# Kernel optimization log

Measured on AMD Instinct MI355X. Metric: run time of the kernel, lower is better.

Reference implementation:

```python
import jax, jax.numpy as jnp
import numpy as np

C = 256        # channels per FPN level (in_channels == representation_size)
PATCH = 5      # GNN kernel_size == stride
NEG_SLOPE = 0.2
K = 7          # node_connectivities[0]


def _conv1x1(x, w, b):
    return jnp.einsum('bchw,oc->bohw', x, w) + b[None, :, None, None]


def _conv3x3(x, w, b):
    y = jax.lax.conv_general_dilated(x, w, (1, 1), 'SAME',
                                     dimension_numbers=('NCHW', 'OIHW', 'NCHW'))
    return y + b[None, :, None, None]


def _nearest(x, hout, wout):
    hin, win = x.shape[-2:]
    ih = (jnp.arange(hout) * hin) // hout
    iw = (jnp.arange(wout) * win) // wout
    return x[..., ih, :][..., iw]


def _topk_edges(score, k, n):
    # torch: A.scatter(1, topk_idx, topk_val); edge = nonzero(triu(A)); edge=[col,row]
    vals, idx = jax.lax.top_k(score, k)          # per-row top-k
    row = jnp.repeat(jnp.arange(n), k)
    col = idx.reshape(-1)
    val = vals.reshape(-1)
    # triu keeps col>=row; GATv2Conv removes self loops then re-adds one per node
    mask = (col > row) & (val != 0.0)
    loop = jnp.arange(n)
    src = jnp.concatenate([col, loop])           # PyG edge_index[0] = source
    dst = jnp.concatenate([row, loop])
    emask = jnp.concatenate([mask, jnp.ones((n,), bool)])
    return src, dst, emask


def _gatv2(x, src, dst, emask, wl, bl, wr, br, att, bias, n):
    heads, dout = att.shape
    xl = (x @ wl + bl).reshape(n, heads, dout)   # source transform (lin_l)
    xr = (x @ wr + br).reshape(n, heads, dout)   # target transform (lin_r)
    m = xl[src] + xr[dst]                        # [E, H, D]
    e = jnp.sum(jax.nn.leaky_relu(m, NEG_SLOPE) * att[None], axis=-1)  # [E, H]
    e = jnp.where(emask[:, None], e, -1e30)
    emax = jax.ops.segment_max(e, dst, num_segments=n)
    w = jnp.exp(e - emax[dst]) * emask[:, None]
    denom = jax.ops.segment_sum(w, dst, num_segments=n)
    alpha = w / (denom[dst] + 1e-16)
    out = jax.ops.segment_sum(alpha[..., None] * xl[src], dst, num_segments=n)
    return out.reshape(n, heads * dout) + bias


def _gnn(x, p, k):
    # x: [1, C, H, W], H,W divisible by PATCH
    _, c, hh, ww = x.shape
    nh, nw = hh // PATCH, ww // PATCH
    n = nh * nw
    patches = x[0].reshape(c, nh, PATCH, nw, PATCH).transpose(1, 3, 0, 2, 4)
    patches = patches.reshape(n, c, PATCH, PATCH)
    emb = jax.nn.relu(jnp.einsum('ncij,ocij->no', patches, p['conv1_w']) + p['conv1_b'])
    emb = jax.nn.relu(emb @ p['fc2_w'].T + p['fc2_b'])
    # feature-similarity kNN graph
    src, dst, em = _topk_edges(emb @ emb.T, k, n)
    h = jax.nn.elu(_gatv2(emb, src, dst, em, *p['g1'], n))
    h = jax.nn.elu(_gatv2(h, src, dst, em, *p['g2'], n))
    # spatial kNN graph (k smallest distances; self distance 0 drops out via val!=0)
    ii, jj = jnp.meshgrid(jnp.arange(nh) * PATCH, jnp.arange(nw) * PATCH, indexing='ij')
    centers = jnp.stack([ii.reshape(-1), jj.reshape(-1)], -1).astype(x.dtype)
    dist = jnp.sqrt(jnp.sum((centers[:, None] - centers[None]) ** 2, -1))
    src2, dst2, em2 = _topk_edges(-dist, k, n)
    h2 = jax.nn.elu(_gatv2(emb, src2, dst2, em2, *p['g3'], n))
    h2 = jax.nn.elu(_gatv2(h2, src2, dst2, em2, *p['g4'], n))
    hc = jax.nn.relu(jnp.concatenate([h, h2], 1) @ p['fc3_w'].T + p['fc3_b']) + h2
    # torch: reshape(dim,dim,C).swapdims(-1,0) -> [C, nw, nh]
    grid = jnp.transpose(hc.reshape(nh, nw, c), (2, 1, 0))
    # ConvTranspose2d(C, C, 5, stride=5): non-overlapping tiling
    up = jnp.einsum('cij,coab->oiajb', grid, p['convT_w'])
    up = up.reshape(c, nw * PATCH, nh * PATCH) + p['convT_b'][:, None, None]
    return jax.nn.relu(up)[None]


def _forward(feat0, feat1, inner_w, inner_b, layer_w, layer_b, convT_w, convT_b,
             conv1_w, conv1_b, fc2_w, fc2_b, fc3_w, fc3_b,
             g1_wl, g1_bl, g1_wr, g1_br, g1_att, g1_bias,
             g2_wl, g2_bl, g2_wr, g2_br, g2_att, g2_bias,
             g3_wl, g3_bl, g3_wr, g3_br, g3_att, g3_bias,
             g4_wl, g4_bl, g4_wr, g4_br, g4_att, g4_bias, k):
    feats = [feat0, feat1]
    xs = []
    for i, f in enumerate(feats):
        p = dict(conv1_w=conv1_w[i], conv1_b=conv1_b[i],
                 fc2_w=fc2_w[i], fc2_b=fc2_b[i],
                 fc3_w=fc3_w[i], fc3_b=fc3_b[i],
                 convT_w=convT_w[i], convT_b=convT_b[i],
                 g1=(g1_wl[i], g1_bl[i], g1_wr[i], g1_br[i], g1_att[i], g1_bias[i]),
                 g2=(g2_wl[i], g2_bl[i], g2_wr[i], g2_br[i], g2_att[i], g2_bias[i]),
                 g3=(g3_wl[i], g3_bl[i], g3_wr[i], g3_br[i], g3_att[i], g3_bias[i]),
                 g4=(g4_wl[i], g4_bl[i], g4_wr[i], g4_br[i], g4_att[i], g4_bias[i]))
        xs.append(f + _gnn(f, p, k))
    # top-down FPN
    last = _conv1x1(xs[1], inner_w[1], inner_b[1])
    out1 = _conv3x3(last, layer_w[1], layer_b[1])
    inner0 = _conv1x1(xs[0], inner_w[0], inner_b[0])
    td = _nearest(last, xs[0].shape[-2], xs[0].shape[-1])
    out0 = _conv3x3(inner0 + td, layer_w[0], layer_b[0])
    return out0, out1


def setup_inputs() -> dict:
    key = jax.random.key(0)
    keys = jax.random.split(key, 48)
    it = iter(range(48))
    def rn(shape, s=0.05):
        return (jax.random.normal(keys[next(it)], shape) * s).astype(jnp.float32)
    H8 = 8 * C
    inp = dict(
        feat0=rn((1, C, 200, 200), 1.0),
        feat1=rn((1, C, 100, 100), 1.0),
        inner_w=rn((2, C, C)), inner_b=rn((2, C)),
        layer_w=rn((2, C, C, 3, 3)), layer_b=rn((2, C)),
        convT_w=rn((2, C, C, PATCH, PATCH)), convT_b=rn((2, C)),
        conv1_w=rn((2, C, C, PATCH, PATCH)), conv1_b=rn((2, C)),
        fc2_w=rn((2, C, C)), fc2_b=rn((2, C)),
        fc3_w=rn((2, C, 2 * C)), fc3_b=rn((2, C)),
        g1_wl=rn((2, C, H8)), g1_bl=rn((2, H8)), g1_wr=rn((2, C, H8)), g1_br=rn((2, H8)),
        g1_att=rn((2, 8, C)), g1_bias=rn((2, H8)),
        g2_wl=rn((2, H8, C)), g2_bl=rn((2, C)), g2_wr=rn((2, H8, C)), g2_br=rn((2, C)),
        g2_att=rn((2, 1, C)), g2_bias=rn((2, C)),
        g3_wl=rn((2, C, H8)), g3_bl=rn((2, H8)), g3_wr=rn((2, C, H8)), g3_br=rn((2, H8)),
        g3_att=rn((2, 8, C)), g3_bias=rn((2, H8)),
        g4_wl=rn((2, H8, C)), g4_bl=rn((2, C)), g4_wr=rn((2, H8, C)), g4_br=rn((2, C)),
        g4_att=rn((2, 1, C)), g4_bias=rn((2, C)),
        k=K,
    )
    return inp


def reference(feat0, feat1, inner_w, inner_b, layer_w, layer_b, convT_w, convT_b,
              conv1_w, conv1_b, fc2_w, fc2_b, fc3_w, fc3_b,
              g1_wl, g1_bl, g1_wr, g1_br, g1_att, g1_bias,
              g2_wl, g2_bl, g2_wr, g2_br, g2_att, g2_bias,
              g3_wl, g3_bl, g3_wr, g3_br, g3_att, g3_bias,
              g4_wl, g4_bl, g4_wr, g4_br, g4_att, g4_bias, k):
    return _forward(feat0, feat1, inner_w, inner_b, layer_w, layer_b, convT_w, convT_b,
                    conv1_w, conv1_b, fc2_w, fc2_b, fc3_w, fc3_b,
                    g1_wl, g1_bl, g1_wr, g1_br, g1_att, g1_bias,
                    g2_wl, g2_bl, g2_wr, g2_br, g2_att, g2_bias,
                    g3_wl, g3_bl, g3_wr, g3_br, g3_att, g3_bias,
                    g4_wl, g4_bl, g4_wr, g4_br, g4_att, g4_bias, k)
```

## Files before the change

### kernel.cpp

```cpp
#include <hip/hip_runtime.h>
#include <cstdint>
#include <cstddef>
#include <math.h>

#define KNN 7

using short8  = __attribute__((ext_vector_type(8))) short;
using floatx4 = __attribute__((ext_vector_type(4))) float;

static const size_t OFF_ARENA = 0;
static const size_t OFF_XS0   = 10240000;
static const size_t OFF_XS1   = 20480000;
static const size_t OFF_LAST  = 23040000;
static const size_t OFF_EMB   = 25600000;
static const size_t OFF_EMB2  = 26009600;
static const size_t OFF_XL    = 26419200;
static const size_t OFF_H1    = 32972800;
static const size_t OFF_XL2   = 36249600;
static const size_t OFF_CAT   = 37068800;
static const size_t OFF_HC    = 37888000;
static const size_t OFF_SRCF  = 38400000;
static const size_t OFF_SRCS  = 38411200;
static const size_t OFF_BF_A  = 38422400;
static const size_t OFF_BF_W  = 40122400;

static __device__ __forceinline__ unsigned short f2bf(float f) {
    union { float f; unsigned u; } v; v.f = f;
    unsigned u = v.u;
    unsigned r = u + 0x7fffu + ((u >> 16) & 1u);
    return (unsigned short)(r >> 16);
}

template<int ACT, bool BIAS>
__global__ __launch_bounds__(256)
void gemm_k(const float* __restrict__ A, const float* __restrict__ B,
            const float* __restrict__ bias, float* __restrict__ C, int M, int N, int K)
{
    __shared__ float As[16][68];
    __shared__ float Bs[16][68];
    const int tid = threadIdx.x;
    const int bm0 = blockIdx.y * 64;
    const int bn0 = blockIdx.x * 64;
    const int tx = tid & 15, ty = tid >> 4;
    const int lrow = tid >> 2;
    const int lk4  = (tid & 3) << 2;
    const int m = bm0 + lrow;
    const int nn = bn0 + lrow;
    const bool aok = m < M, bok = nn < N;
    float acc[4][4] = {{0.f,0.f,0.f,0.f},{0.f,0.f,0.f,0.f},{0.f,0.f,0.f,0.f},{0.f,0.f,0.f,0.f}};

    float4 va = {0.f,0.f,0.f,0.f}, vb = {0.f,0.f,0.f,0.f};
    if (aok) va = *(const float4*)(A + (size_t)m * K + lk4);
    if (bok) vb = *(const float4*)(B + (size_t)nn * K + lk4);

    for (int k0 = 0; k0 < K; k0 += 16) {
        As[lk4+0][lrow]=va.x; As[lk4+1][lrow]=va.y; As[lk4+2][lrow]=va.z; As[lk4+3][lrow]=va.w;
        Bs[lk4+0][lrow]=vb.x; Bs[lk4+1][lrow]=vb.y; Bs[lk4+2][lrow]=vb.z; Bs[lk4+3][lrow]=vb.w;
        __syncthreads();
        float4 na = {0.f,0.f,0.f,0.f}, nb = {0.f,0.f,0.f,0.f};
        const bool more = (k0 + 16) < K;
        if (more) {
            if (aok) na = *(const float4*)(A + (size_t)m * K + (k0 + 16 + lk4));
            if (bok) nb = *(const float4*)(B + (size_t)nn * K + (k0 + 16 + lk4));
        }
        #pragma unroll
        for (int k = 0; k < 16; k++) {
            const float4 av = *(const float4*)&As[k][ty << 2];
            const float4 bv = *(const float4*)&Bs[k][tx << 2];
            const float a0=av.x,a1=av.y,a2=av.z,a3=av.w;
            const float b0=bv.x,b1=bv.y,b2=bv.z,b3=bv.w;
            acc[0][0]=fmaf(a0,b0,acc[0][0]); acc[0][1]=fmaf(a0,b1,acc[0][1]);
            acc[0][2]=fmaf(a0,b2,acc[0][2]); acc[0][3]=fmaf(a0,b3,acc[0][3]);
            acc[1][0]=fmaf(a1,b0,acc[1][0]); acc[1][1]=fmaf(a1,b1,acc[1][1]);
            acc[1][2]=fmaf(a1,b2,acc[1][2]); acc[1][3]=fmaf(a1,b3,acc[1][3]);
            acc[2][0]=fmaf(a2,b0,acc[2][0]); acc[2][1]=fmaf(a2,b1,acc[2][1]);
            acc[2][2]=fmaf(a2,b2,acc[2][2]); acc[2][3]=fmaf(a2,b3,acc[2][3]);
            acc[3][0]=fmaf(a3,b0,acc[3][0]); acc[3][1]=fmaf(a3,b1,acc[3][1]);
            acc[3][2]=fmaf(a3,b2,acc[3][2]); acc[3][3]=fmaf(a3,b3,acc[3][3]);
        }
        __syncthreads();
        va = na; vb = nb;
    }
    #pragma unroll
    for (int i = 0; i < 4; i++) {
        const int mm = bm0 + (ty << 2) + i;
        if (mm >= M) continue;
        #pragma unroll
        for (int jj = 0; jj < 4; jj++) {
            const int nc = bn0 + (tx << 2) + jj;
            if (nc >= N) continue;
            float v = acc[i][jj];
            if (BIAS) v += bias[nc];
            if (ACT == 1) v = fmaxf(v, 0.f);
            C[(size_t)mm * N + nc] = v;
        }
    }
}

template<int ACT, bool BIAS>
static inline void gemm32(hipStream_t s, const float* A, const float* B, const float* bias,
                          float* C, int M, int N, int K)
{
    dim3 g((N + 63) / 64, (M + 63) / 64);
    gemm_k<ACT, BIAS><<<g, dim3(256), 0, s>>>(A, B, bias, C, M, N, K);
}

__global__ __launch_bounds__(256)
void gemm32_sk_k(const float* __restrict__ A, const float* __restrict__ B,
                 float* __restrict__ part, int M, int N, int K, int Kc)
{
    __shared__ float As[16][68];
    __shared__ float Bs[16][68];
    const int tid = threadIdx.x;
    const int bm0 = blockIdx.y * 64;
    const int bn0 = blockIdx.x * 64;
    const int sblk = blockIdx.z;
    const int kbeg = sblk * Kc;
    const int kend = (kbeg + Kc < K) ? kbeg + Kc : K;
    const int tx = tid & 15, ty = tid >> 4;
    const int lrow = tid >> 2;
    const int lk4  = (tid & 3) << 2;
    const int m = bm0 + lrow;
    const int nn = bn0 + lrow;
    const bool aok = m < M, bok = nn < N;
    float acc[4][4] = {{0.f,0.f,0.f,0.f},{0.f,0.f,0.f,0.f},{0.f,0.f,0.f,0.f},{0.f,0.f,0.f,0.f}};

    float4 va = {0.f,0.f,0.f,0.f}, vb = {0.f,0.f,0.f,0.f};
    if (aok) va = *(const float4*)(A + (size_t)m * K + kbeg + lk4);
    if (bok) vb = *(const float4*)(B + (size_t)nn * K + kbeg + lk4);

    for (int k0 = kbeg; k0 < kend; k0 += 16) {
        As[lk4+0][lrow]=va.x; As[lk4+1][lrow]=va.y; As[lk4+2][lrow]=va.z; As[lk4+3][lrow]=va.w;
        Bs[lk4+0][lrow]=vb.x; Bs[lk4+1][lrow]=vb.y; Bs[lk4+2][lrow]=vb.z; Bs[lk4+3][lrow]=vb.w;
        __syncthreads();
        float4 na = {0.f,0.f,0.f,0.f}, nb = {0.f,0.f,0.f,0.f};
        const bool more = (k0 + 16) < kend;
        if (more) {
            if (aok) na = *(const float4*)(A + (size_t)m * K + (k0 + 16 + lk4));
            if (bok) nb = *(const float4*)(B + (size_t)nn * K + (k0 + 16 + lk4));
        }
        #pragma unroll
        for (int k = 0; k < 16; k++) {
            const float4 av = *(const float4*)&As[k][ty << 2];
            const float4 bv = *(const float4*)&Bs[k][tx << 2];
            const float a0=av.x,a1=av.y,a2=av.z,a3=av.w;
            const float b0=bv.x,b1=bv.y,b2=bv.z,b3=bv.w;
            acc[0][0]=fmaf(a0,b0,acc[0][0]); acc[0][1]=fmaf(a0,b1,acc[0][1]);
            acc[0][2]=fmaf(a0,b2,acc[0][2]); acc[0][3]=fmaf(a0,b3,acc[0][3]);
            acc[1][0]=fmaf(a1,b0,acc[1][0]); acc[1][1]=fmaf(a1,b1,acc[1][1]);
            acc[1][2]=fmaf(a1,b2,acc[1][2]); acc[1][3]=fmaf(a1,b3,acc[1][3]);
            acc[2][0]=fmaf(a2,b0,acc[2][0]); acc[2][1]=fmaf(a2,b1,acc[2][1]);
            acc[2][2]=fmaf(a2,b2,acc[2][2]); acc[2][3]=fmaf(a2,b3,acc[2][3]);
            acc[3][0]=fmaf(a3,b0,acc[3][0]); acc[3][1]=fmaf(a3,b1,acc[3][1]);
            acc[3][2]=fmaf(a3,b2,acc[3][2]); acc[3][3]=fmaf(a3,b3,acc[3][3]);
        }
        __syncthreads();
        va = na; vb = nb;
    }
    float* P = part + (size_t)sblk * M * N;
    #pragma unroll
    for (int i = 0; i < 4; i++) {
        const int mm = bm0 + (ty << 2) + i;
        if (mm >= M) continue;
        #pragma unroll
        for (int jj = 0; jj < 4; jj++) {
            const int nc = bn0 + (tx << 2) + jj;
            if (nc >= N) continue;
            P[(size_t)mm * N + nc] = acc[i][jj];
        }
    }
}

template<int ACT, bool BIAS>
__global__ void sk_reduce_k(const float* __restrict__ part, const float* __restrict__ bias,
                            float* __restrict__ C, int MN, int N, int S)
{
    const int i4 = (blockIdx.x * 256 + threadIdx.x) * 4;
    if (i4 >= MN) return;
    float4 a = *(const float4*)(part + i4);
    for (int s = 1; s < S; s++) {
        const float4 b = *(const float4*)(part + (size_t)s * MN + i4);
        a.x += b.x; a.y += b.y; a.z += b.z; a.w += b.w;
    }
    if (BIAS) {
        const int n = i4 % N;
        a.x += bias[n]; a.y += bias[n + 1]; a.z += bias[n + 2]; a.w += bias[n + 3];
    }
    if (ACT == 1) {
        a.x = fmaxf(a.x, 0.f); a.y = fmaxf(a.y, 0.f);
        a.z = fmaxf(a.z, 0.f); a.w = fmaxf(a.w, 0.f);
    }
    *(float4*)(C + i4) = a;
}

template<int ACT, bool BIAS>
static inline void gemm32_sk(hipStream_t s, const float* A, const float* B, const float* bias,
                             float* C, float* part, int M, int N, int K, int S)
{
    const int Kc = ((K / S + 15) / 16) * 16;
    dim3 g((N + 63) / 64, (M + 63) / 64, S);
    gemm32_sk_k<<<g, dim3(256), 0, s>>>(A, B, part, M, N, K, Kc);
    const int MN = M * N;
    sk_reduce_k<ACT, BIAS><<<dim3((MN / 4 + 255) / 256), dim3(256), 0, s>>>(part, bias, C, MN, N, S);
}

enum { BT_NT = 0, BT_CONV2 = 2 };

template<int BT, int ACT, int BAX, bool ADDMAT>
__global__ __launch_bounds__(256)
void bgemm_k(const unsigned short* __restrict__ A, const unsigned short* __restrict__ B,
             const float* __restrict__ bias, const float* __restrict__ bias2, int nsplit,
             const float* __restrict__ Dmat, int Dld,
             float* __restrict__ C, int M, int N, int K, int imH, int imW)
{
    __shared__ unsigned short Asl[128][40];
    __shared__ unsigned short Bsl[128][40];
    const int tid  = threadIdx.x;
    const int lane = tid & 63;
    const int wid  = tid >> 6;
    const int quad = lane >> 4;
    const int l15  = lane & 15;
    const int wy = wid >> 1, wx = wid & 1;
    const int bm0 = blockIdx.y * 128;
    const int bn0 = blockIdx.x * 128;

    floatx4 zero = {0.f, 0.f, 0.f, 0.f};
    floatx4 acc[4][4];
    #pragma unroll
    for (int i = 0; i < 4; i++)
        #pragma unroll
        for (int j = 0; j < 4; j++) acc[i][j] = zero;

    const int srow = tid >> 1;
    const int skc  = (tid & 1) << 4;
    const int mrow = bm0 + srow;
    const bool aok = mrow < M;
    const int nrow = bn0 + srow;
    const bool bok = nrow < N;

    int cy = 0, cx = 0; bool cok = false;
    if (BT == BT_CONV2) {
        cok = nrow < N;
        const int pp = cok ? nrow : 0;
        cy = pp / imW; cx = pp - cy * imW;
    }

    auto loadA = [&](int k0, uint4& r0, uint4& r1) {
        r0 = (uint4){0,0,0,0}; r1 = (uint4){0,0,0,0};
        if (aok) {
            const uint4* p = (const uint4*)(A + (size_t)mrow * K + k0 + skc);
            r0 = p[0]; r1 = p[1];
        }
    };
    auto loadB = [&](int k0, uint4& r0, uint4& r1) {
        r0 = (uint4){0,0,0,0}; r1 = (uint4){0,0,0,0};
        if (BT == BT_NT) {
            if (bok) {
                const uint4* p = (const uint4*)(B + (size_t)nrow * K + k0 + skc);
                r0 = p[0]; r1 = p[1];
            }
        } else {
            const int jj = k0 >> 8;
            const int j3 = jj / 3;
            const int dy = j3 - 1, dx = jj - j3 * 3 - 1;
            const int c0 = k0 & 255;
            const int yy = cy + dy, xx = cx + dx;
            if (cok && (unsigned)yy < (unsigned)imH && (unsigned)xx < (unsigned)imW) {
                const uint4* p = (const uint4*)(B + ((size_t)yy * imW + xx) * 256 + c0 + skc);
                r0 = p[0]; r1 = p[1];
            }
        }
    };
    auto stage = [&](const uint4& a0, const uint4& a1, const uint4& b0, const uint4& b1) {
        *(uint4*)&Asl[srow][skc]     = a0;
        *(uint4*)&Asl[srow][skc + 8] = a1;
        *(uint4*)&Bsl[srow][skc]     = b0;
        *(uint4*)&Bsl[srow][skc + 8] = b1;
    };
    auto compute = [&]() {
        short8 af[4], bfr[4];
        #pragma unroll
        for (int i = 0; i < 4; i++)
            af[i] = *(const short8*)&Asl[wy * 64 + i * 16 + l15][quad * 8];
        #pragma unroll
        for (int j = 0; j < 4; j++)
            bfr[j] = *(const short8*)&Bsl[wx * 64 + j * 16 + l15][quad * 8];
        #pragma unroll
        for (int i = 0; i < 4; i++)
            #pragma unroll
            for (int j = 0; j < 4; j++)
                acc[i][j] = __builtin_amdgcn_mfma_f32_16x16x32_bf16(af[i], bfr[j], acc[i][j], 0, 0, 0);
    };

    uint4 a00, a01, b00, b01, a10, a11, b10, b11;
    loadA(0, a00, a01); loadB(0, b00, b01);
    if (32 < K) { loadA(32, a10, a11); loadB(32, b10, b11); }

    for (int k0 = 0; k0 < K; k0 += 64) {
        stage(a00, a01, b00, b01);
        __syncthreads();
        if (k0 + 64 < K) { loadA(k0 + 64, a00, a01); loadB(k0 + 64, b00, b01); }
        compute();
        __syncthreads();
        if (k0 + 32 < K) {
            stage(a10, a11, b10, b11);
            __syncthreads();
            if (k0 + 96 < K) { loadA(k0 + 96, a10, a11); loadB(k0 + 96, b10, b11); }
            compute();
            __syncthreads();
        }
    }

    #pragma unroll
    for (int i = 0; i < 4; i++) {
        #pragma unroll
        for (int r = 0; r < 4; r++) {
            const int m = bm0 + wy * 64 + i * 16 + quad * 4 + r;
            if (m >= M) continue;
            #pragma unroll
            for (int j = 0; j < 4; j++) {
                const int n = bn0 + wx * 64 + j * 16 + l15;
                if (n >= N) continue;
                float v = acc[i][j][r];
                if (bias != nullptr)
                    v += (BAX == 0) ? bias[m] : (n < nsplit ? bias[n] : bias2[n - nsplit]);
                if (ACT == 1) v = fmaxf(v, 0.f);
                if (ADDMAT) v += Dmat[(size_t)m * Dld + n];
                C[(size_t)m * N + n] = v;
            }
        }
    }
}

template<int BT, int ACT, int BAX, bool ADDMAT>
static inline void bgemm(hipStream_t s, const unsigned short* A, const unsigned short* B,
                         const float* bias, const float* bias2, int nsplit,
                         const float* D, int Dld, float* C,
                         int M, int N, int K, int imH = 0, int imW = 0)
{
    dim3 g((N + 127) / 128, (M + 127) / 128);
    bgemm_k<BT, ACT, BAX, ADDMAT><<<g, dim3(256), 0, s>>>(A, B, bias, bias2, nsplit,
                                                          D, Dld, C, M, N, K, imH, imW);
}

__global__ __launch_bounds__(256)
void bgemm_sk_k(const unsigned short* __restrict__ A, const unsigned short* __restrict__ B,
                float* __restrict__ part, int M, int N, int K, int Kc)
{
    __shared__ unsigned short Asl[128][40];
    __shared__ unsigned short Bsl[128][40];
    const int tid  = threadIdx.x;
    const int lane = tid & 63;
    const int wid  = tid >> 6;
    const int quad = lane >> 4;
    const int l15  = lane & 15;
    const int wy = wid >> 1, wx = wid & 1;
    const int bm0 = blockIdx.y * 128;
    const int bn0 = blockIdx.x * 128;
    const int kbeg = blockIdx.z * Kc;
    const int kend = (kbeg + Kc < K) ? kbeg + Kc : K;

    floatx4 zero = {0.f, 0.f, 0.f, 0.f};
    floatx4 acc[4][4];
    #pragma unroll
    for (int i = 0; i < 4; i++)
        #pragma unroll
        for (int j = 0; j < 4; j++) acc[i][j] = zero;

    const int srow = tid >> 1;
    const int skc  = (tid & 1) << 4;
    const int mrow = bm0 + srow;
    const bool aok = mrow < M;
    const int nrow = bn0 + srow;
    const bool bok = nrow < N;

    auto loadA = [&](int k0, uint4& r0, uint4& r1) {
        r0 = (uint4){0,0,0,0}; r1 = (uint4){0,0,0,0};
        if (aok) {
            const uint4* p = (const uint4*)(A + (size_t)mrow * K + k0 + skc);
            r0 = p[0]; r1 = p[1];
        }
    };
    auto loadB = [&](int k0, uint4& r0, uint4& r1) {
        r0 = (uint4){0,0,0,0}; r1 = (uint4){0,0,0,0};
        if (bok) {
            const uint4* p = (const uint4*)(B + (size_t)nrow * K + k0 + skc);
            r0 = p[0]; r1 = p[1];
        }
    };
    auto stage = [&](const uint4& a0, const uint4& a1, const uint4& b0, const uint4& b1) {
        *(uint4*)&Asl[srow][skc]     = a0;
        *(uint4*)&Asl[srow][skc + 8] = a1;
        *(uint4*)&Bsl[srow][skc]     = b0;
        *(uint4*)&Bsl[srow][skc + 8] = b1;
    };
    auto compute = [&]() {
        short8 af[4], bfr[4];
        #pragma unroll
        for (int i = 0; i < 4; i++)
            af[i] = *(const short8*)&Asl[wy * 64 + i * 16 + l15][quad * 8];
        #pragma unroll
        for (int j = 0; j < 4; j++)
            bfr[j] = *(const short8*)&Bsl[wx * 64 + j * 16 + l15][quad * 8];
        #pragma unroll
        for (int i = 0; i < 4; i++)
            #pragma unroll
            for (int j = 0; j < 4; j++)
                acc[i][j] = __builtin_amdgcn_mfma_f32_16x16x32_bf16(af[i], bfr[j], acc[i][j], 0, 0, 0);
    };

    uint4 a00, a01, b00, b01, a10, a11, b10, b11;
    loadA(kbeg, a00, a01); loadB(kbeg, b00, b01);
    if (kbeg + 32 < kend) { loadA(kbeg + 32, a10, a11); loadB(kbeg + 32, b10, b11); }

    for (int k0 = kbeg; k0 < kend; k0 += 64) {
        stage(a00, a01, b00, b01);
        __syncthreads();
        if (k0 + 64 < kend) { loadA(k0 + 64, a00, a01); loadB(k0 + 64, b00, b01); }
        compute();
        __syncthreads();
        if (k0 + 32 < kend) {
            stage(a10, a11, b10, b11);
            __syncthreads();
            if (k0 + 96 < kend) { loadA(k0 + 96, a10, a11); loadB(k0 + 96, b10, b11); }
            compute();
            __syncthreads();
        }
    }

    float* P = part + (size_t)blockIdx.z * M * N;
    #pragma unroll
    for (int i = 0; i < 4; i++) {
        #pragma unroll
        for (int r = 0; r < 4; r++) {
            const int m = bm0 + wy * 64 + i * 16 + quad * 4 + r;
            if (m >= M) continue;
            #pragma unroll
            for (int j = 0; j < 4; j++) {
                const int n = bn0 + wx * 64 + j * 16 + l15;
                if (n >= N) continue;
                P[(size_t)m * N + n] = acc[i][j][r];
            }
        }
    }
}

template<int ACT, bool ADDMAT>
__global__ void bsk_reduce_k(const float* __restrict__ part,
                             const float* __restrict__ bias, const float* __restrict__ bias2,
                             int nsplit, const float* __restrict__ Dmat, int Dld,
                             float* __restrict__ C, int MN, int N, int S)
{
    const int i4 = (blockIdx.x * 256 + threadIdx.x) * 4;
    if (i4 >= MN) return;
    float4 a = *(const float4*)(part + i4);
    for (int s = 1; s < S; s++) {
        const float4 b = *(const float4*)(part + (size_t)s * MN + i4);
        a.x += b.x; a.y += b.y; a.z += b.z; a.w += b.w;
    }
    const int n = i4 % N;
    const float* bb = (n < nsplit) ? (bias + n) : (bias2 + n - nsplit);
    a.x += bb[0]; a.y += bb[1]; a.z += bb[2]; a.w += bb[3];
    if (ACT == 1) {
        a.x = fmaxf(a.x, 0.f); a.y = fmaxf(a.y, 0.f);
        a.z = fmaxf(a.z, 0.f); a.w = fmaxf(a.w, 0.f);
    }
    if (ADDMAT) {
        const int m = i4 / N;
        const float4 d = *(const float4*)(Dmat + (size_t)m * Dld + n);
        a.x += d.x; a.y += d.y; a.z += d.z; a.w += d.w;
    }
    *(float4*)(C + i4) = a;
}

template<int ACT, bool ADDMAT>
static inline void bgemm_sk(hipStream_t s, const unsigned short* A, const unsigned short* B,
                            const float* bias, const float* bias2, int nsplit,
                            const float* D, int Dld, float* C, float* part,
                            int M, int N, int K, int S)
{
    const int Kc = ((K / S + 31) / 32) * 32;
    dim3 g((N + 127) / 128, (M + 127) / 128, S);
    bgemm_sk_k<<<g, dim3(256), 0, s>>>(A, B, part, M, N, K, Kc);
    const int MN = M * N;
    bsk_reduce_k<ACT, ADDMAT><<<dim3((MN / 4 + 255) / 256), dim3(256), 0, s>>>(
        part, bias, bias2, nsplit, D, Dld, C, MN, N, S);
}

__global__ void cast_bf16_k(const float* __restrict__ in, unsigned short* __restrict__ out, int total)
{
    const int i4 = (blockIdx.x * 256 + threadIdx.x) * 4;
    if (i4 + 4 <= total) {
        const float4 v = *(const float4*)(in + i4);
        ushort4 o;
        o.x = f2bf(v.x); o.y = f2bf(v.y); o.z = f2bf(v.z); o.w = f2bf(v.w);
        *(ushort4*)(out + i4) = o;
    } else {
        for (int i = i4; i < total; i++) out[i] = f2bf(in[i]);
    }
}

static inline void cast_bf(hipStream_t s, const float* in, unsigned short* out, int total)
{
    cast_bf16_k<<<dim3((total / 4 + 255) / 256), dim3(256), 0, s>>>(in, out, total);
}

__device__ __forceinline__ void cast_t_body(const float* __restrict__ in,
                                            unsigned short* __restrict__ out, int K, int N)
{
    __shared__ float tile[64][65];
    const int n0 = blockIdx.x * 64;
    const int k0 = blockIdx.y * 64;
    const int t = threadIdx.x;
    const int r = t >> 2;
    const int c4 = (t & 3) << 4;
    {
        const int k = k0 + r;
        if (k < K && n0 + c4 + 16 <= N) {
            const float4* p = (const float4*)(in + (size_t)k * N + n0 + c4);
            *(float4*)&tile[r][c4]      = p[0];
            *(float4*)&tile[r][c4 + 4]  = p[1];
            *(float4*)&tile[r][c4 + 8]  = p[2];
            *(float4*)&tile[r][c4 + 12] = p[3];
        } else {
            for (int i = 0; i < 16; i++)
                tile[r][c4 + i] = (k < K && n0 + c4 + i < N) ? in[(size_t)k * N + n0 + c4 + i] : 0.f;
        }
    }
    __syncthreads();
    const int n = n0 + r;
    if (n >= N) return;
    unsigned short tmp[16];
    #pragma unroll
    for (int i = 0; i < 16; i++) tmp[i] = f2bf(tile[c4 + i][r]);
    if (k0 + 64 <= K) {
        *(uint4*)(out + (size_t)n * K + k0 + c4)     = *(uint4*)&tmp[0];
        *(uint4*)(out + (size_t)n * K + k0 + c4 + 8) = *(uint4*)&tmp[8];
    } else {
        for (int i = 0; i < 16; i++)
            if (k0 + c4 + i < K) out[(size_t)n * K + k0 + c4 + i] = tmp[i];
    }
}

__global__ void cast_t_k(const float* __restrict__ in, unsigned short* __restrict__ out, int K, int N)
{
    cast_t_body(in, out, K, N);
}

__global__ void cast_t2_k(const float* __restrict__ in0, const float* __restrict__ in1,
                          unsigned short* __restrict__ out0, unsigned short* __restrict__ out1,
                          int K, int N)
{
    if (blockIdx.z == 0) cast_t_body(in0, out0, K, N);
    else                 cast_t_body(in1, out1, K, N);
}

static inline void cast_t(hipStream_t s, const float* in, unsigned short* out, int K, int N)
{
    cast_t_k<<<dim3((N + 63) / 64, (K + 63) / 64), dim3(256), 0, s>>>(in, out, K, N);
}

static inline void cast_t2(hipStream_t s, const float* in0, const float* in1,
                           unsigned short* out0, unsigned short* out1, int K, int N)
{
    cast_t2_k<<<dim3((N + 63) / 64, (K + 63) / 64, 2), dim3(256), 0, s>>>(in0, in1, out0, out1, K, N);
}

__global__ void reorder_w3_k(const float* __restrict__ in, unsigned short* __restrict__ out)
{
    const int idx = blockIdx.x * 256 + threadIdx.x;
    if (idx >= 589824) return;
    const int o = idx / 2304;
    const int r = idx - o * 2304;
    const int j = r >> 8;
    const int c = r & 255;
    out[idx] = f2bf(in[(size_t)o * 2304 + c * 9 + j]);
}

__global__ void extract_patches_k(const float* __restrict__ f, float* __restrict__ patches,
                                  int nw, int H, int total)
{
    int idx = blockIdx.x * 256 + threadIdx.x;
    if (idx >= total) return;
    int q = idx % 6400;
    int p = idx / 6400;
    int c = q / 25;
    int rem = q - c * 25;
    int a = rem / 5, b = rem - (rem / 5) * 5;
    int ih = p / nw, iw = p - (p / nw) * nw;
    patches[idx] = f[(size_t)c * H * H + (size_t)(ih * 5 + a) * H + (iw * 5 + b)];
}

__global__ void topk_feat_k(const float* __restrict__ score, int* __restrict__ srcCols, int n)
{
    const int r = blockIdx.x;
    const int lane = threadIdx.x;
    const float* row = score + (size_t)r * n;
    int   sel[KNN];
    float selv[KNN];
    #pragma unroll
    for (int t = 0; t < KNN; t++) {
        float best = -__builtin_huge_valf();
        int   bidx = 0x7fffffff;
        for (int c = lane; c < n; c += 64) {
            bool taken = false;
            #pragma unroll
            for (int u = 0; u < KNN; u++)
                if (u < t && sel[u] == c) taken = true;
            if (taken) continue;
            float v = row[c];
            if (v > best || (v == best && c < bidx)) { best = v; bidx = c; }
        }
        #pragma unroll
        for (int off = 32; off > 0; off >>= 1) {
            float ov = __shfl_down(best, off);
            int   oi = __shfl_down(bidx, off);
            if (ov > best || (ov == best && oi < bidx)) { best = ov; bidx = oi; }
        }
        best = __shfl(best, 0);
        bidx = __shfl(bidx, 0);
        sel[t] = bidx; selv[t] = best;
    }
    if (lane < KNN) {
        int c = -1; float v = 0.f;
        #pragma unroll
        for (int t = 0; t < KNN; t++)
            if (lane == t) { c = sel[t]; v = selv[t]; }
        srcCols[r * KNN + lane] = (c > r && v != 0.0f) ? c : -1;
    }
}

__global__ void topk_spatial_k(int* __restrict__ srcCols, int n, int nw)
{
    const int r = blockIdx.x;
    const int lane = threadIdx.x;
    const int ri = r / nw, rj = r - (r / nw) * nw;
    int sel[KNN];
    #pragma unroll
    for (int t = 0; t < KNN; t++) {
        int bkey = 0x7fffffff;
        for (int c = lane; c < n; c += 64) {
            bool taken = false;
            #pragma unroll
            for (int u = 0; u < KNN; u++)
                if (u < t && sel[u] == c) taken = true;
            if (taken) continue;
            const int ci = c / nw, cj = c - (c / nw) * nw;
            const int dy = (ri - ci) * 5, dx = (rj - cj) * 5;
            const int d2 = dy * dy + dx * dx;
            const int key = (d2 << 11) | c;
            if (key < bkey) bkey = key;
        }
        #pragma unroll
        for (int off = 32; off > 0; off >>= 1) {
            int ok = __shfl_down(bkey, off);
            if (ok < bkey) bkey = ok;
        }
        bkey = __shfl(bkey, 0);
        sel[t] = bkey & 2047;
    }
    if (lane < KNN) {
        int c = -1;
        #pragma unroll
        for (int t = 0; t < KNN; t++) if (lane == t) c = sel[t];
        srcCols[r * KNN + lane] = (c > r) ? c : -1;
    }
}

__global__ void gat_fused_k(const float* __restrict__ x, int xroff, int xstride,
                            const float* __restrict__ att,
                            const int* __restrict__ srcCols, const float* __restrict__ bias,
                            float* __restrict__ out, int n, int H, int ostride, int ooff)
{
    const int wid = (blockIdx.x * blockDim.x + threadIdx.x) >> 6;
    const int lane = threadIdx.x & 63;
    if (wid >= n * H) return;
    const int h = wid % H;
    const int r = wid / H;
    const int d0 = lane << 2;

    const float4 xrf  = *(const float4*)(x + (size_t)r * xstride + xroff + h * 256 + d0);
    const float4 attf = *(const float4*)(att + (size_t)h * 256 + d0);

    int srcs[8];
    #pragma unroll
    for (int s_ = 0; s_ < KNN; s_++) srcs[s_] = srcCols[r * KNN + s_];
    srcs[7] = r;

    float4 xlf[8];
    float  e[8];
    #pragma unroll
    for (int s_ = 0; s_ < 8; s_++) {
        const int c = srcs[s_];
        float4 v = {0.f, 0.f, 0.f, 0.f};
        if (c >= 0) v = *(const float4*)(x + (size_t)c * xstride + h * 256 + d0);
        xlf[s_] = v;
        float m, p = 0.f;
        m = v.x + xrf.x; m = (m > 0.f) ? m : 0.2f * m; p += m * attf.x;
        m = v.y + xrf.y; m = (m > 0.f) ? m : 0.2f * m; p += m * attf.y;
        m = v.z + xrf.z; m = (m > 0.f) ? m : 0.2f * m; p += m * attf.z;
        m = v.w + xrf.w; m = (m > 0.f) ? m : 0.2f * m; p += m * attf.w;
        #pragma unroll
        for (int off = 32; off > 0; off >>= 1) p += __shfl_down(p, off);
        e[s_] = __shfl(p, 0);
    }

    float mx = e[7];
    #pragma unroll
    for (int s_ = 0; s_ < KNN; s_++)
        if (srcs[s_] >= 0) mx = fmaxf(mx, e[s_]);
    float a[8], denom = 0.f;
    #pragma unroll
    for (int s_ = 0; s_ < 8; s_++) {
        a[s_] = (s_ == 7 || srcs[s_] >= 0) ? expf(e[s_] - mx) : 0.f;
        denom += a[s_];
    }
    const float inv = 1.f / (denom + 1e-16f);

    float o0 = 0.f, o1 = 0.f, o2 = 0.f, o3 = 0.f;
    #pragma unroll
    for (int s_ = 0; s_ < 8; s_++) {
        const float al = a[s_] * inv;
        o0 = fmaf(al, xlf[s_].x, o0); o1 = fmaf(al, xlf[s_].y, o1);
        o2 = fmaf(al, xlf[s_].z, o2); o3 = fmaf(al, xlf[s_].w, o3);
    }
    const float* bb = bias + (size_t)h * 256 + d0;
    o0 += bb[0]; o1 += bb[1]; o2 += bb[2]; o3 += bb[3];
    o0 = (o0 > 0.f) ? o0 : (expf(o0) - 1.f);
    o1 = (o1 > 0.f) ? o1 : (expf(o1) - 1.f);
    o2 = (o2 > 0.f) ? o2 : (expf(o2) - 1.f);
    o3 = (o3 > 0.f) ? o3 : (expf(o3) - 1.f);
    float4 res = {o0, o1, o2, o3};
    *(float4*)(out + (size_t)r * ostride + ooff + (size_t)h * 256 + d0) = res;
}

__global__ void scatter_convT_k(const float* __restrict__ f, const float* __restrict__ U,
                                const float* __restrict__ bias, float* __restrict__ xs,
                                int nw, int H, int total)
{
    int idx = blockIdx.x * 256 + threadIdx.x;
    if (idx >= total) return;
    int x = idx % H;
    int t = idx / H;
    int y = t % H;
    int o = t / H;
    int j = y / 5, a = y - j * 5;
    int i = x / 5, b = x - i * 5;
    int p = i * nw + j;
    float v = U[(size_t)p * 6400 + o * 25 + a * 5 + b] + bias[o];
    v = fmaxf(v, 0.f);
    xs[idx] = f[idx] + v;
}

__global__ void upsample_add_k(float* __restrict__ acc, const float* __restrict__ last,
                               int H, int Hs, int total)
{
    int idx = blockIdx.x * 256 + threadIdx.x;
    if (idx >= total) return;
    int x = idx % H;
    int t = idx / H;
    int y = t % H;
    int c = t / H;
    acc[idx] += last[(size_t)c * Hs * Hs + (size_t)(y >> 1) * Hs + (x >> 1)];
}

static void run_level(void* const* d_in, float* ws, int l, int H, hipStream_t s)
{
    const float* f = (const float*)d_in[l];
    const int nh = H / 5, nw = nh, n = nh * nw, HW = H * H;

    const float* convT_w = (const float*)d_in[6]  + (size_t)l * 1638400;
    const float* convT_b = (const float*)d_in[7]  + l * 256;
    const float* conv1_w = (const float*)d_in[8]  + (size_t)l * 1638400;
    const float* conv1_b = (const float*)d_in[9]  + l * 256;
    const float* fc2_w   = (const float*)d_in[10] + (size_t)l * 65536;
    const float* fc2_b   = (const float*)d_in[11] + l * 256;
    const float* fc3_w   = (const float*)d_in[12] + (size_t)l * 131072;
    const float* fc3_b   = (const float*)d_in[13] + l * 256;
    const float* g1_wl   = (const float*)d_in[14] + (size_t)l * 524288;
    const float* g1_bl   = (const float*)d_in[15] + l * 2048;
    const float* g1_wr   = (const float*)d_in[16] + (size_t)l * 524288;
    const float* g1_br   = (const float*)d_in[17] + l * 2048;
    const float* g1_att  = (const float*)d_in[18] + l * 2048;
    const float* g1_bias = (const float*)d_in[19] + l * 2048;
    const float* g2_wl   = (const float*)d_in[20] + (size_t)l * 524288;
    const float* g2_bl   = (const float*)d_in[21] + l * 256;
    const float* g2_wr   = (const float*)d_in[22] + (size_t)l * 524288;
    const float* g2_br   = (const float*)d_in[23] + l * 256;
    const float* g2_att  = (const float*)d_in[24] + l * 256;
    const float* g2_bias = (const float*)d_in[25] + l * 256;
    const float* g3_wl   = (const float*)d_in[26] + (size_t)l * 524288;
    const float* g3_bl   = (const float*)d_in[27] + l * 2048;
    const float* g3_wr   = (const float*)d_in[28] + (size_t)l * 524288;
    const float* g3_br   = (const float*)d_in[29] + l * 2048;
    const float* g3_att  = (const float*)d_in[30] + l * 2048;
    const float* g3_bias = (const float*)d_in[31] + l * 2048;
    const float* g4_wl   = (const float*)d_in[32] + (size_t)l * 524288;
    const float* g4_bl   = (const float*)d_in[33] + l * 256;
    const float* g4_wr   = (const float*)d_in[34] + (size_t)l * 524288;
    const float* g4_br   = (const float*)d_in[35] + l * 256;
    const float* g4_att  = (const float*)d_in[36] + l * 256;
    const float* g4_bias = (const float*)d_in[37] + l * 256;

    float* patches = ws + OFF_ARENA;
    float* xs    = ws + (l == 0 ? OFF_XS0 : OFF_XS1);
    float* emb   = ws + OFF_EMB;
    float* emb2  = ws + OFF_EMB2;
    float* score = ws + OFF_LAST;
    float* xlr   = ws + OFF_XL;
    float* h1    = ws + OFF_H1;
    float* xlr2  = ws + OFF_XL2;
    float* cat   = ws + OFF_CAT;
    float* hc    = ws + OFF_HC;
    int* srcF = (int*)(ws + OFF_SRCF);
    int* srcS = (int*)(ws + OFF_SRCS);
    unsigned short* ba = (unsigned short*)(ws + OFF_BF_A);
    unsigned short* bw = (unsigned short*)(ws + OFF_BF_W);
    float* part = ws + OFF_ARENA;

    { int tot = n * 6400;
      extract_patches_k<<<dim3((tot + 255) / 256), dim3(256), 0, s>>>(f, patches, nw, H, tot); }

    gemm32_sk<1, true>(s, patches, conv1_w, conv1_b, emb, xlr, n, 256, 6400, 16);
    gemm32<1, true>(s, emb, fc2_w, fc2_b, emb2, n, 256, 256);
    gemm32<0, false>(s, emb2, emb2, nullptr, score, n, n, 256);
    topk_feat_k<<<dim3(n), dim3(64), 0, s>>>(score, srcF, n);
    topk_spatial_k<<<dim3(n), dim3(64), 0, s>>>(srcS, n, nw);

    const int gatw1 = n * 8;
    const int gatw2 = n;

    cast_bf(s, emb2, ba, n * 256);
    cast_t2(s, g1_wl, g1_wr, bw, bw + 2048 * 256, 256, 2048);
    if (n >= 1024)
        bgemm<BT_NT, 0, 1, false>(s, ba, bw, g1_bl, g1_br, 2048, nullptr, 0, xlr, n, 4096, 256);
    else
        bgemm_sk<0, false>(s, ba, bw, g1_bl, g1_br, 2048, nullptr, 0, xlr, part, n, 4096, 256, 2);
    gat_fused_k<<<dim3((gatw1 + 3) / 4), dim3(256), 0, s>>>(xlr, 2048, 4096, g1_att, srcF, g1_bias, h1, n, 8, 2048, 0);

    cast_bf(s, h1, ba, n * 2048);
    cast_t2(s, g2_wl, g2_wr, bw, bw + 256 * 2048, 2048, 256);
    bgemm_sk<0, false>(s, ba, bw, g2_bl, g2_br, 256, nullptr, 0, xlr2, part, n, 512, 2048, 8);
    gat_fused_k<<<dim3((gatw2 + 3) / 4), dim3(256), 0, s>>>(xlr2, 256, 512, g2_att, srcF, g2_bias, cat, n, 1, 512, 0);

    cast_bf(s, emb2, ba, n * 256);
    cast_t2(s, g3_wl, g3_wr, bw, bw + 2048 * 256, 256, 2048);
    if (n >= 1024)
        bgemm<BT_NT, 0, 1, false>(s, ba, bw, g3_bl, g3_br, 2048, nullptr, 0, xlr, n, 4096, 256);
    else
        bgemm_sk<0, false>(s, ba, bw, g3_bl, g3_br, 2048, nullptr, 0, xlr, part, n, 4096, 256, 2);
    gat_fused_k<<<dim3((gatw1 + 3) / 4), dim3(256), 0, s>>>(xlr, 2048, 4096, g3_att, srcS, g3_bias, h1, n, 8, 2048, 0);

    cast_bf(s, h1, ba, n * 2048);
    cast_t2(s, g4_wl, g4_wr, bw, bw + 256 * 2048, 2048, 256);
    bgemm_sk<0, false>(s, ba, bw, g4_bl, g4_br, 256, nullptr, 0, xlr2, part, n, 512, 2048, 8);
    gat_fused_k<<<dim3((gatw2 + 3) / 4), dim3(256), 0, s>>>(xlr2, 256, 512, g4_att, srcS, g4_bias, cat, n, 1, 512, 256);

    cast_bf(s, cat, ba, n * 512);
    cast_bf(s, fc3_w, bw, 131072);
    bgemm_sk<1, true>(s, ba, bw, fc3_b, fc3_b, 256, cat + 256, 512, hc, part, n, 256, 512, 4);
    cast_bf(s, hc, ba, n * 256);
    cast_t(s, convT_w, bw, 256, 6400);
    bgemm<BT_NT, 0, 1, false>(s, ba, bw, nullptr, nullptr, 0, nullptr, 0, patches, n, 6400, 256);
    { int tot = 256 * HW;
      scatter_convT_k<<<dim3((tot + 255) / 256), dim3(256), 0, s>>>(f, patches, convT_b, xs, nw, H, tot); }
}

extern "C" void kernel_launch(void* const* d_in, const int* in_sizes, int n_in,
                              void* d_out, int out_size, void* d_ws, size_t ws_size,
                              hipStream_t stream)
{
    float* ws  = (float*)d_ws;
    float* out = (float*)d_out;

    run_level(d_in, ws, 0, 200, stream);
    run_level(d_in, ws, 1, 100, stream);

    const float* inner_w = (const float*)d_in[2];
    const float* inner_b = (const float*)d_in[3];
    const float* layer_w = (const float*)d_in[4];
    const float* layer_b = (const float*)d_in[5];
    float* xs0    = ws + OFF_XS0;
    float* xs1    = ws + OFF_XS1;
    float* last   = ws + OFF_LAST;
    float* inner0 = ws + OFF_ARENA;
    unsigned short* bimg = (unsigned short*)(ws + OFF_XL);
    unsigned short* bw1  = (unsigned short*)(ws + OFF_BF_W);
    unsigned short* bwc  = (unsigned short*)(ws + OFF_BF_W + 100000);

    cast_t(stream, xs1, bimg, 256, 10000);
    cast_bf(stream, inner_w + 65536, bw1, 65536);
    bgemm<BT_NT, 0, 0, false>(stream, bw1, bimg, inner_b + 256, nullptr, 0, nullptr, 0,
                              last, 256, 10000, 256);
    reorder_w3_k<<<dim3((589824 + 255) / 256), dim3(256), 0, stream>>>(layer_w + 589824, bwc);
    cast_t(stream, last, bimg, 256, 10000);
    bgemm<BT_CONV2, 0, 0, false>(stream, bwc, bimg, layer_b + 256, nullptr, 0, nullptr, 0,
                                 out + 10240000, 256, 10000, 2304, 100, 100);

    cast_t(stream, xs0, bimg, 256, 40000);
    cast_bf(stream, inner_w, bw1, 65536);
    bgemm<BT_NT, 0, 0, false>(stream, bw1, bimg, inner_b, nullptr, 0, nullptr, 0,
                              inner0, 256, 40000, 256);
    { int tot = 256 * 40000;
      upsample_add_k<<<dim3((tot + 255) / 256), dim3(256), 0, stream>>>(inner0, last, 200, 100, tot); }
    reorder_w3_k<<<dim3((589824 + 255) / 256), dim3(256), 0, stream>>>(layer_w, bwc);
    cast_t(stream, inner0, bimg, 256, 40000);
    bgemm<BT_CONV2, 0, 0, false>(stream, bwc, bimg, layer_b, nullptr, 0, nullptr, 0,
                                 out, 256, 40000, 2304, 200, 200);
}
```

Baseline: 1.268 ms.

## Stage bf16 GEMM tiles via direct global-to-LDS loads with double buffering

Replaces the register-staged global loads and LDS writes in the bf16 MFMA GEMM kernels with global_load_lds async copies into double-buffered shared memory. This cuts the syncs per k-step to one and removes the VGPR round trip for A and B tiles. The conv-im2col B path keeps register loads but now double-buffers its LDS writes. Out-of-range rows are clamped to the last valid row instead of zero-filled, and the unpadded 32-wide LDS rows may cause bank conflicts on MFMA fragment reads. Correctness also relies on the barrier ordering the async LDS writes, with no explicit vmcnt wait.

```diff
diff --git a/kernel.cpp b/kernel.cpp
--- a/kernel.cpp
+++ b/kernel.cpp
@@ -31,6 +31,11 @@
     return (unsigned short)(r >> 16);
 }
 
+static __device__ __forceinline__ void glds16(const void* g, void* l) {
+    __builtin_amdgcn_global_load_lds((const __attribute__((address_space(1))) void*)g,
+                                     (__attribute__((address_space(3))) void*)l, 16, 0, 0);
+}
+
 template<int ACT, bool BIAS>
 __global__ __launch_bounds__(256)
 void gemm_k(const float* __restrict__ A, const float* __restrict__ B,
@@ -206,6 +211,7 @@
 
 enum { BT_NT = 0, BT_CONV2 = 2 };
 
+
 template<int BT, int ACT, int BAX, bool ADDMAT>
 __global__ __launch_bounds__(256)
 void bgemm_k(const unsigned short* __restrict__ A, const unsigned short* __restrict__ B,
@@ -213,8 +219,8 @@
              const float* __restrict__ Dmat, int Dld,
              float* __restrict__ C, int M, int N, int K, int imH, int imW)
 {
-    __shared__ unsigned short Asl[128][40];
-    __shared__ unsigned short Bsl[128][40];
+    __shared__ unsigned short As[2][4096];
+    __shared__ unsigned short Bs[2][4096];
     const int tid  = threadIdx.x;
     const int lane = tid & 63;
     const int wid  = tid >> 6;
@@ -231,60 +237,63 @@
         #pragma unroll
         for (int j = 0; j < 4; j++) acc[i][j] = zero;
 
-    const int srow = tid >> 1;
-    const int skc  = (tid & 1) << 4;
-    const int mrow = bm0 + srow;
-    const bool aok = mrow < M;
-    const int nrow = bn0 + srow;
-    const bool bok = nrow < N;
-
-    int cy = 0, cx = 0; bool cok = false;
+    const int l4 = lane >> 2, sc = lane & 3;
+    const int r0 = wid * 32 + l4;
+    const int r1 = r0 + 16;
+    int am0 = bm0 + r0; if (am0 > M - 1) am0 = M - 1;
+    int am1 = bm0 + r1; if (am1 > M - 1) am1 = M - 1;
+    const unsigned short* aP0 = A + (size_t)am0 * K + sc * 8;
+    const unsigned short* aP1 = A + (size_t)am1 * K + sc * 8;
+
+    const unsigned short* bP0 = A;
+    const unsigned short* bP1 = A;
+    if (BT == BT_NT) {
+        int bn0r = bn0 + r0; if (bn0r > N - 1) bn0r = N - 1;
+        int bn1r = bn0 + r1; if (bn1r > N - 1) bn1r = N - 1;
+        bP0 = B + (size_t)bn0r * K + sc * 8;
+        bP1 = B + (size_t)bn1r * K + sc * 8;
+    }
+
+    const int crow  = tid >> 1;
+    const int chalf = (tid & 1) << 4;
+    int cy = 0, cx = 0;
     if (BT == BT_CONV2) {
-        cok = nrow < N;
-        const int pp = cok ? nrow : 0;
+        int pp = bn0 + crow; if (pp > N - 1) pp = N - 1;
         cy = pp / imW; cx = pp - cy * imW;
     }
 
-    auto loadA = [&](int k0, uint4& r0, uint4& r1) {
-        r0 = (uint4){0,0,0,0}; r1 = (uint4){0,0,0,0};
-        if (aok) {
-            const uint4* p = (const uint4*)(A + (size_t)mrow * K + k0 + skc);
-            r0 = p[0]; r1 = p[1];
-        }
+    auto stageA = [&](int buf, int k0) {
+        glds16(aP0 + k0, &As[buf][(wid * 2 + 0) * 512]);
+        glds16(aP1 + k0, &As[buf][(wid * 2 + 1) * 512]);
     };
-    auto loadB = [&](int k0, uint4& r0, uint4& r1) {
-        r0 = (uint4){0,0,0,0}; r1 = (uint4){0,0,0,0};
-        if (BT == BT_NT) {
-            if (bok) {
-                const uint4* p = (const uint4*)(B + (size_t)nrow * K + k0 + skc);
-                r0 = p[0]; r1 = p[1];
-            }
-        } else {
-            const int jj = k0 >> 8;
-            const int j3 = jj / 3;
-            const int dy = j3 - 1, dx = jj - j3 * 3 - 1;
-            const int c0 = k0 & 255;
-            const int yy = cy + dy, xx = cx + dx;
-            if (cok && (unsigned)yy < (unsigned)imH && (unsigned)xx < (unsigned)imW) {
-                const uint4* p = (const uint4*)(B + ((size_t)yy * imW + xx) * 256 + c0 + skc);
-                r0 = p[0]; r1 = p[1];
-            }
-        }
+    auto stageB = [&](int buf, int k0) {
+        glds16(bP0 + k0, &Bs[buf][(wid * 2 + 0) * 512]);
+        glds16(bP1 + k0, &Bs[buf][(wid * 2 + 1) * 512]);
     };
-    auto stage = [&](const uint4& a0, const uint4& a1, const uint4& b0, const uint4& b1) {
-        *(uint4*)&Asl[srow][skc]     = a0;
-        *(uint4*)&Asl[srow][skc + 8] = a1;
-        *(uint4*)&Bsl[srow][skc]     = b0;
-        *(uint4*)&Bsl[srow][skc + 8] = b1;
+    auto ldB_conv = [&](int k0, uint4& q0, uint4& q1) {
+        const int jj = k0 >> 8;
+        const int j3 = jj / 3;
+        const int dy = j3 - 1, dx = jj - j3 * 3 - 1;
+        const int c0 = k0 & 255;
+        const int yy = cy + dy, xx = cx + dx;
+        q0 = (uint4){0, 0, 0, 0}; q1 = (uint4){0, 0, 0, 0};
+        if ((unsigned)yy < (unsigned)imH && (unsigned)xx < (unsigned)imW) {
+            const uint4* p = (const uint4*)(B + (((size_t)yy * imW + xx) << 8) + c0 + chalf);
+            q0 = p[0]; q1 = p[1];
+        }
     };
-    auto compute = [&]() {
+    auto wrB = [&](int buf, const uint4& q0, const uint4& q1) {
+        *(uint4*)&Bs[buf][crow * 32 + chalf]     = q0;
+        *(uint4*)&Bs[buf][crow * 32 + chalf + 8] = q1;
+    };
+    auto compute = [&](int buf) {
         short8 af[4], bfr[4];
         #pragma unroll
         for (int i = 0; i < 4; i++)
-            af[i] = *(const short8*)&Asl[wy * 64 + i * 16 + l15][quad * 8];
+            af[i] = *(const short8*)&As[buf][(wy * 64 + i * 16 + l15) * 32 + quad * 8];
         #pragma unroll
         for (int j = 0; j < 4; j++)
-            bfr[j] = *(const short8*)&Bsl[wx * 64 + j * 16 + l15][quad * 8];
+            bfr[j] = *(const short8*)&Bs[buf][(wx * 64 + j * 16 + l15) * 32 + quad * 8];
         #pragma unroll
         for (int i = 0; i < 4; i++)
             #pragma unroll
@@ -292,22 +301,31 @@
                 acc[i][j] = __builtin_amdgcn_mfma_f32_16x16x32_bf16(af[i], bfr[j], acc[i][j], 0, 0, 0);
     };
 
-    uint4 a00, a01, b00, b01, a10, a11, b10, b11;
-    loadA(0, a00, a01); loadB(0, b00, b01);
-    if (32 < K) { loadA(32, a10, a11); loadB(32, b10, b11); }
-
-    for (int k0 = 0; k0 < K; k0 += 64) {
-        stage(a00, a01, b00, b01);
-        __syncthreads();
-        if (k0 + 64 < K) { loadA(k0 + 64, a00, a01); loadB(k0 + 64, b00, b01); }
-        compute();
-        __syncthreads();
-        if (k0 + 32 < K) {
-            stage(a10, a11, b10, b11);
+    if (BT == BT_NT) {
+        stageA(0, 0); stageB(0, 0);
+        int bufc = 0;
+        for (int k0 = 0; k0 < K; k0 += 32) {
             __syncthreads();
-            if (k0 + 96 < K) { loadA(k0 + 96, a10, a11); loadB(k0 + 96, b10, b11); }
-            compute();
+            if (k0 + 32 < K) { stageA(bufc ^ 1, k0 + 32); stageB(bufc ^ 1, k0 + 32); }
+            compute(bufc);
+            bufc ^= 1;
+        }
+    } else {
+        uint4 b00, b01, b10, b11;
+        ldB_conv(0, b00, b01);
+        if (32 < K) ldB_conv(32, b10, b11);
+        stageA(0, 0); wrB(0, b00, b01);
+        for (int k0 = 0; k0 < K; k0 += 64) {
             __syncthreads();
+            if (k0 + 64 < K) ldB_conv(k0 + 64, b00, b01);
+            if (k0 + 32 < K) { stageA(1, k0 + 32); wrB(1, b10, b11); }
+            compute(0);
+            if (k0 + 32 < K) {
+                __syncthreads();
+                if (k0 + 96 < K) ldB_conv(k0 + 96, b10, b11);
+                if (k0 + 64 < K) { stageA(0, k0 + 64); wrB(0, b00, b01); }
+                compute(1);
+            }
         }
     }
 
@@ -347,8 +365,8 @@
 void bgemm_sk_k(const unsigned short* __restrict__ A, const unsigned short* __restrict__ B,
                 float* __restrict__ part, int M, int N, int K, int Kc)
 {
-    __shared__ unsigned short Asl[128][40];
-    __shared__ unsigned short Bsl[128][40];
+    __shared__ unsigned short As[2][4096];
+    __shared__ unsigned short Bs[2][4096];
     const int tid  = threadIdx.x;
     const int lane = tid & 63;
     const int wid  = tid >> 6;
@@ -367,41 +385,34 @@
         #pragma unroll
         for (int j = 0; j < 4; j++) acc[i][j] = zero;
 
-    const int srow = tid >> 1;
-    const int skc  = (tid & 1) << 4;
-    const int mrow = bm0 + srow;
-    const bool aok = mrow < M;
-    const int nrow = bn0 + srow;
-    const bool bok = nrow < N;
-
-    auto loadA = [&](int k0, uint4& r0, uint4& r1) {
-        r0 = (uint4){0,0,0,0}; r1 = (uint4){0,0,0,0};
-        if (aok) {
-            const uint4* p = (const uint4*)(A + (size_t)mrow * K + k0 + skc);
-            r0 = p[0]; r1 = p[1];
-        }
+    const int l4 = lane >> 2, sc = lane & 3;
+    const int r0 = wid * 32 + l4;
+    const int r1 = r0 + 16;
+    int am0 = bm0 + r0; if (am0 > M - 1) am0 = M - 1;
+    int am1 = bm0 + r1; if (am1 > M - 1) am1 = M - 1;
+    int bn0r = bn0 + r0; if (bn0r > N - 1) bn0r = N - 1;
+    int bn1r = bn0 + r1; if (bn1r > N - 1) bn1r = N - 1;
+    const unsigned short* aP0 = A + (size_t)am0 * K + sc * 8;
+    const unsigned short* aP1 = A + (size_t)am1 * K + sc * 8;
+    const unsigned short* bP0 = B + (size_t)bn0r * K + sc * 8;
+    const unsigned short* bP1 = B + (size_t)bn1r * K + sc * 8;
+
+    auto stageA = [&](int buf, int k0) {
+        glds16(aP0 + k0, &As[buf][(wid * 2 + 0) * 512]);
+        glds16(aP1 + k0, &As[buf][(wid * 2 + 1) * 512]);
     };
-    auto loadB = [&](int k0, uint4& r0, uint4& r1) {
-        r0 = (uint4){0,0,0,0}; r1 = (uint4){0,0,0,0};
-        if (bok) {
-            const uint4* p = (const uint4*)(B + (size_t)nrow * K + k0 + skc);
-            r0 = p[0]; r1 = p[1];
-        }
+    auto stageB = [&](int buf, int k0) {
+        glds16(bP0 + k0, &Bs[buf][(wid * 2 + 0) * 512]);
+        glds16(bP1 + k0, &Bs[buf][(wid * 2 + 1) * 512]);
     };
-    auto stage = [&](const uint4& a0, const uint4& a1, const uint4& b0, const uint4& b1) {
-        *(uint4*)&Asl[srow][skc]     = a0;
-        *(uint4*)&Asl[srow][skc + 8] = a1;
-        *(uint4*)&Bsl[srow][skc]     = b0;
-        *(uint4*)&Bsl[srow][skc + 8] = b1;
-    };
-    auto compute = [&]() {
+    auto compute = [&](int buf) {
         short8 af[4], bfr[4];
         #pragma unroll
         for (int i = 0; i < 4; i++)
-            af[i] = *(const short8*)&Asl[wy * 64 + i * 16 + l15][quad * 8];
+            af[i] = *(const short8*)&As[buf][(wy * 64 + i * 16 + l15) * 32 + quad * 8];
         #pragma unroll
         for (int j = 0; j < 4; j++)
-            bfr[j] = *(const short8*)&Bsl[wx * 64 + j * 16 + l15][quad * 8];
+            bfr[j] = *(const short8*)&Bs[buf][(wx * 64 + j * 16 + l15) * 32 + quad * 8];
         #pragma unroll
         for (int i = 0; i < 4; i++)
             #pragma unroll
@@ -409,23 +420,13 @@
                 acc[i][j] = __builtin_amdgcn_mfma_f32_16x16x32_bf16(af[i], bfr[j], acc[i][j], 0, 0, 0);
     };
 
-    uint4 a00, a01, b00, b01, a10, a11, b10, b11;
-    loadA(kbeg, a00, a01); loadB(kbeg, b00, b01);
-    if (kbeg + 32 < kend) { loadA(kbeg + 32, a10, a11); loadB(kbeg + 32, b10, b11); }
-
-    for (int k0 = kbeg; k0 < kend; k0 += 64) {
-        stage(a00, a01, b00, b01);
+    stageA(0, kbeg); stageB(0, kbeg);
+    int bufc = 0;
+    for (int k0 = kbeg; k0 < kend; k0 += 32) {
         __syncthreads();
-        if (k0 + 64 < kend) { loadA(k0 + 64, a00, a01); loadB(k0 + 64, b00, b01); }
-        compute();
-        __syncthreads();
-        if (k0 + 32 < kend) {
-            stage(a10, a11, b10, b11);
-            __syncthreads();
-            if (k0 + 96 < kend) { loadA(k0 + 96, a10, a11); loadB(k0 + 96, b10, b11); }
-            compute();
-            __syncthreads();
-        }
+        if (k0 + 32 < kend) { stageA(bufc ^ 1, k0 + 32); stageB(bufc ^ 1, k0 + 32); }
+        compute(bufc);
+        bufc ^= 1;
     }
 
     float* P = part + (size_t)blockIdx.z * M * N;
```

New measurement: 1.231 ms. -2.9%, faster.
